# Optimization experiments

Measured on AMD Instinct MI355X. Metric: run time of the kernel, lower is better.

Reference implementation:

```python
import jax, jax.numpy as jnp
import numpy as np

N_HEAD, D_HEAD, D_MODEL = 8, 64, 512
QLEN, MLEN, BSZ = 1024, 1024, 4
KLEN = QLEN + MLEN
SCALE = 1.0 / (D_HEAD ** 0.5)
LN_EPS = 1e-5


def _rel_shift(x):
    # x: [qlen, rlen, bsz, n_head]
    q, rl, b, n = x.shape
    zero_pad = jnp.zeros((q, 1, b, n), x.dtype)
    x_padded = jnp.concatenate([zero_pad, x], axis=1).reshape(rl + 1, q, b, n)
    return x_padded[1:].reshape(q, rl, b, n)


def _layer_norm(x, g, b):
    mu = jnp.mean(x, axis=-1, keepdims=True)
    var = jnp.var(x, axis=-1, keepdims=True)
    return (x - mu) * jax.lax.rsqrt(var + LN_EPS) * g + b


def setup_inputs() -> dict:
    key = jax.random.key(0)
    ks = jax.random.split(key, 10)
    s = 0.02
    return {
        "w": jax.random.normal(ks[0], (QLEN, BSZ, D_MODEL), jnp.float32),
        "r": jax.random.normal(ks[1], (KLEN, 1, D_MODEL), jnp.float32),
        "r_w_bias": jax.random.normal(ks[2], (N_HEAD, D_HEAD), jnp.float32) * s,
        "r_r_bias": jax.random.normal(ks[3], (N_HEAD, D_HEAD), jnp.float32) * s,
        "mems": jax.random.normal(ks[4], (MLEN, BSZ, D_MODEL), jnp.float32),
        "Wq": jax.random.normal(ks[5], (D_MODEL, N_HEAD * D_HEAD), jnp.float32) * s,
        "Wkv": jax.random.normal(ks[6], (D_MODEL, 2 * N_HEAD * D_HEAD), jnp.float32) * s,
        "Wr": jax.random.normal(ks[7], (D_MODEL, N_HEAD * D_HEAD), jnp.float32) * s,
        "Wo": jax.random.normal(ks[8], (N_HEAD * D_HEAD, D_MODEL), jnp.float32) * s,
        "ln_g": jnp.ones((D_MODEL,), jnp.float32),
        "ln_b": jnp.zeros((D_MODEL,), jnp.float32),
        # causal mask: query i can attend keys j <= i + MLEN
        "attn_mask": jnp.arange(KLEN)[None, :] > (jnp.arange(QLEN) + MLEN)[:, None],
    }


def reference(w, r, r_w_bias, r_r_bias, mems, Wq, Wkv, Wr, Wo, ln_g, ln_b, attn_mask):
    qlen, bsz = w.shape[0], w.shape[1]
    cat = jnp.concatenate([mems, w], axis=0)          # [klen, bsz, d_model]
    klen = cat.shape[0]

    r_head_k = (r[:, 0] @ Wr).reshape(-1, N_HEAD, D_HEAD)   # [rlen, n, d]
    kv = cat @ Wkv                                           # [klen, bsz, 2*n*d]
    w_head_k, w_head_v = jnp.split(kv, 2, axis=-1)
    w_head_q = (cat[-qlen:] @ Wq).reshape(qlen, bsz, N_HEAD, D_HEAD)
    w_head_k = w_head_k.reshape(klen, bsz, N_HEAD, D_HEAD)
    w_head_v = w_head_v.reshape(klen, bsz, N_HEAD, D_HEAD)

    AC = jnp.einsum('ibnd,jbnd->ijbn', w_head_q + r_w_bias, w_head_k)
    BD = jnp.einsum('ibnd,jnd->ijbn', w_head_q + r_r_bias, r_head_k)
    BD = _rel_shift(BD)[:, :klen]

    attn_score = (AC + BD) * SCALE                           # [qlen, klen, bsz, n]
    attn_score = jnp.where(attn_mask[:, :, None, None], -jnp.inf, attn_score)
    attn_prob = jax.nn.softmax(attn_score, axis=1)

    attn_vec = jnp.einsum('ijbn,jbnd->ibnd', attn_prob, w_head_v)
    attn_vec = attn_vec.reshape(qlen, bsz, N_HEAD * D_HEAD)
    attn_out = attn_vec @ Wo
    return _layer_norm(w + attn_out, ln_g, ln_b)
```

## Files before the change

### kernel.cpp

```cpp
#include <hip/hip_runtime.h>
#include <hip/hip_bf16.h>
#include <math.h>

#define QLEN 1024
#define MLEN 1024
#define KLEN 2048
#define BSZ 4
#define NH 8
#define DH 64
#define DM 512
#define SCALE 0.125f
#define LN_EPS 1e-5f

#define RK_ROWS 2112

typedef __attribute__((ext_vector_type(8))) short short8;
typedef __attribute__((ext_vector_type(4))) float float4_;

#define GLB(p) ((const __attribute__((address_space(1))) void*)(p))
#define LDSP(p) ((__attribute__((address_space(3))) void*)(p))

__device__ inline ushort to_bf16(float x) {
  __hip_bfloat16 h = __float2bfloat16(x);
  return *reinterpret_cast<ushort*>(&h);
}

__device__ inline float row_max16(float v) {
  int x = __builtin_bit_cast(int, v);
  v = fmaxf(v, __builtin_bit_cast(float, __builtin_amdgcn_update_dpp(x, x, 0xB1, 0xF, 0xF, false)));
  x = __builtin_bit_cast(int, v);
  v = fmaxf(v, __builtin_bit_cast(float, __builtin_amdgcn_update_dpp(x, x, 0x4E, 0xF, 0xF, false)));
  x = __builtin_bit_cast(int, v);
  v = fmaxf(v, __builtin_bit_cast(float, __builtin_amdgcn_update_dpp(x, x, 0x124, 0xF, 0xF, false)));
  x = __builtin_bit_cast(int, v);
  v = fmaxf(v, __builtin_bit_cast(float, __builtin_amdgcn_update_dpp(x, x, 0x128, 0xF, 0xF, false)));
  return v;
}
__device__ inline float row_sum16(float v) {
  int x = __builtin_bit_cast(int, v);
  v += __builtin_bit_cast(float, __builtin_amdgcn_update_dpp(x, x, 0xB1, 0xF, 0xF, false));
  x = __builtin_bit_cast(int, v);
  v += __builtin_bit_cast(float, __builtin_amdgcn_update_dpp(x, x, 0x4E, 0xF, 0xF, false));
  x = __builtin_bit_cast(int, v);
  v += __builtin_bit_cast(float, __builtin_amdgcn_update_dpp(x, x, 0x124, 0xF, 0xF, false));
  x = __builtin_bit_cast(int, v);
  v += __builtin_bit_cast(float, __builtin_amdgcn_update_dpp(x, x, 0x128, 0xF, 0xF, false));
  return v;
}

__global__ __launch_bounds__(256) void wtrans_all(
    const float* __restrict__ Wq, const float* __restrict__ Wkv,
    const float* __restrict__ Wr, const float* __restrict__ Wo,
    ushort* __restrict__ WqT, ushort* __restrict__ WkvT,
    ushort* __restrict__ WrT, ushort* __restrict__ WoT) {
  __shared__ ushort tile[32][33];
  const int z = blockIdx.z;
  const float* W;
  ushort* WT;
  int N;
  if (z == 0)      { W = Wq;  WT = WqT;  N = DM; }
  else if (z == 1) { W = Wkv; WT = WkvT; N = 2 * DM; }
  else if (z == 2) { W = Wr;  WT = WrT;  N = DM; }
  else             { W = Wo;  WT = WoT;  N = DM; }
  const int k0 = blockIdx.x * 32, n0 = blockIdx.y * 32;
  if (n0 >= N) return;
  const int tid = threadIdx.x;
#pragma unroll
  for (int it = 0; it < 4; ++it) {
    int idx = tid + it * 256;
    int r = idx >> 5, c = idx & 31;
    tile[r][c] = to_bf16(W[(size_t)(k0 + r) * N + n0 + c]);
  }
  __syncthreads();
#pragma unroll
  for (int it = 0; it < 4; ++it) {
    int idx = tid + it * 256;
    int r = idx >> 5, c = idx & 31;
    WT[(size_t)(n0 + r) * DM + k0 + c] = tile[c][r];
  }
}

__global__ __launch_bounds__(256) void proj_all(
    const float* __restrict__ w, const float* __restrict__ mems,
    const float* __restrict__ r,
    const ushort* __restrict__ WqT, const ushort* __restrict__ WkvT,
    const ushort* __restrict__ WrT,
    const float* __restrict__ bias0, const float* __restrict__ bias1,
    ushort* __restrict__ qw, ushort* __restrict__ qr,
    ushort* __restrict__ k2, ushort* __restrict__ v2,
    ushort* __restrict__ rk2) {
  __shared__ ushort As[128 * 32];
  __shared__ ushort Bs[128 * 32];
  const int tid = threadIdx.x;
  int mode, bx, by;
  {
    int id = blockIdx.x;
    if (id < 128)      { mode = 0; bx = id >> 2;         by = id & 3; }
    else if (id < 640) { mode = 1; bx = (id - 128) >> 3; by = (id - 128) & 7; }
    else               { mode = 2; bx = (id - 640) >> 2; by = (id - 640) & 3; }
  }
  const int m0 = bx * 128, n0 = by * 128;
  const int wv = tid >> 6, lane = tid & 63;
  const int wm = wv >> 1, wn = wv & 1;
  const int l16 = lane & 15, quad = lane >> 4;

  const int arow = tid >> 1;
  const int acol = (tid & 1) * 16;
  const float* asrc;
  {
    int m = m0 + arow;
    if (mode == 2) asrc = r + (size_t)m * DM;
    else asrc = (m < QLEN * BSZ) ? w + (size_t)m * DM
                                 : mems + (size_t)(m - QLEN * BSZ) * DM;
    asrc += acol;
  }
  const ushort* BT = (mode == 0) ? WqT : (mode == 1) ? WkvT : WrT;
  const ushort* bsrc = BT + (size_t)(n0 + arow) * DM + acol;

  float4_ acc[4][4];
#pragma unroll
  for (int a = 0; a < 4; ++a)
#pragma unroll
    for (int b = 0; b < 4; ++b) acc[a][b] = float4_{0.f, 0.f, 0.f, 0.f};

  for (int k0 = 0; k0 < DM; k0 += 32) {
    float4 a0 = *reinterpret_cast<const float4*>(asrc + k0);
    float4 a1 = *reinterpret_cast<const float4*>(asrc + k0 + 4);
    float4 a2 = *reinterpret_cast<const float4*>(asrc + k0 + 8);
    float4 a3 = *reinterpret_cast<const float4*>(asrc + k0 + 12);
    ushort4 u0, u1, u2, u3;
    u0.x = to_bf16(a0.x); u0.y = to_bf16(a0.y); u0.z = to_bf16(a0.z); u0.w = to_bf16(a0.w);
    u1.x = to_bf16(a1.x); u1.y = to_bf16(a1.y); u1.z = to_bf16(a1.z); u1.w = to_bf16(a1.w);
    u2.x = to_bf16(a2.x); u2.y = to_bf16(a2.y); u2.z = to_bf16(a2.z); u2.w = to_bf16(a2.w);
    u3.x = to_bf16(a3.x); u3.y = to_bf16(a3.y); u3.z = to_bf16(a3.z); u3.w = to_bf16(a3.w);
    *reinterpret_cast<ushort4*>(&As[arow * 32 + acol]) = u0;
    *reinterpret_cast<ushort4*>(&As[arow * 32 + acol + 4]) = u1;
    *reinterpret_cast<ushort4*>(&As[arow * 32 + acol + 8]) = u2;
    *reinterpret_cast<ushort4*>(&As[arow * 32 + acol + 12]) = u3;
    *reinterpret_cast<uint4*>(&Bs[arow * 32 + acol]) =
        *reinterpret_cast<const uint4*>(bsrc + k0);
    *reinterpret_cast<uint4*>(&Bs[arow * 32 + acol + 8]) =
        *reinterpret_cast<const uint4*>(bsrc + k0 + 8);
    __syncthreads();
    short8 af[4], bf[4];
#pragma unroll
    for (int f = 0; f < 4; ++f) {
      af[f] = *reinterpret_cast<const short8*>(&As[(wm * 64 + f * 16 + l16) * 32 + quad * 8]);
      bf[f] = *reinterpret_cast<const short8*>(&Bs[(wn * 64 + f * 16 + l16) * 32 + quad * 8]);
    }
#pragma unroll
    for (int fm = 0; fm < 4; ++fm)
#pragma unroll
      for (int fn = 0; fn < 4; ++fn)
        acc[fm][fn] = __builtin_amdgcn_mfma_f32_16x16x32_bf16(bf[fn], af[fm], acc[fm][fn], 0, 0, 0);
    __syncthreads();
  }

#pragma unroll
  for (int fm = 0; fm < 4; ++fm) {
#pragma unroll
    for (int fn = 0; fn < 4; ++fn) {
      const int mm = m0 + wm * 64 + fm * 16 + l16;
      const int nnb = n0 + wn * 64 + fn * 16 + quad * 4;
      const float4_ a = acc[fm][fn];
      if (mode == 0) {
        float4 b0v = *reinterpret_cast<const float4*>(bias0 + nnb);
        float4 b1v = *reinterpret_cast<const float4*>(bias1 + nnb);
        int i = mm >> 2, b = mm & 3;
        int hd = nnb >> 6, d0 = nnb & 63;
        size_t idx = (((size_t)(b * NH + hd)) * QLEN + i) * DH + d0;
        ushort4 o0, o1;
        o0.x = to_bf16(a[0] + b0v.x); o0.y = to_bf16(a[1] + b0v.y);
        o0.z = to_bf16(a[2] + b0v.z); o0.w = to_bf16(a[3] + b0v.w);
        o1.x = to_bf16(a[0] + b1v.x); o1.y = to_bf16(a[1] + b1v.y);
        o1.z = to_bf16(a[2] + b1v.z); o1.w = to_bf16(a[3] + b1v.w);
        *reinterpret_cast<ushort4*>(qw + idx) = o0;
        *reinterpret_cast<ushort4*>(qr + idx) = o1;
      } else if (mode == 1) {
        int pos = mm >> 2, b = mm & 3;
        int jb = pos >> 5, jj = pos & 31;
        if (nnb < DM) {
          int hd = nnb >> 6, d = nnb & 63;
          int bn = b * NH + hd;
          int tile = ((jj >> 4) << 1) | (d >> 5);
          int lane2 = (((d >> 3) & 3) << 4) | (jj & 15);
          ushort4 o;
          o.x = to_bf16(a[0]); o.y = to_bf16(a[1]);
          o.z = to_bf16(a[2]); o.w = to_bf16(a[3]);
          *reinterpret_cast<ushort4*>(
              k2 + ((((size_t)bn * 64 + jb) * 4 + tile) * 64 + lane2) * 8 + (d & 7)) = o;
        } else {
          int nn2 = nnb - DM;
          int hd = nn2 >> 6, d = nn2 & 63;
          int bn = b * NH + hd;
          int tile = d >> 4;
          size_t base = ((((size_t)bn * 64 + jb) * 4 + tile) * 64 +
                         ((jj >> 3) << 4)) * 8 + (jj & 7);
#pragma unroll
          for (int reg = 0; reg < 4; ++reg)
            v2[base + (size_t)((d & 15) + reg) * 8] = to_bf16(a[reg]);
        }
      } else {
        int t = mm;
        int hd = nnb >> 6, d = nnb & 63;
        int cb = d >> 3;
        int dcol = ((cb ^ (t & 7)) << 3) | (d & 7);
        ushort4 o;
        o.x = to_bf16(a[0]); o.y = to_bf16(a[1]);
        o.z = to_bf16(a[2]); o.w = to_bf16(a[3]);
        *reinterpret_cast<ushort4*>(
            rk2 + ((size_t)hd * RK_ROWS + t) * DH + dcol) = o;
      }
    }
  }
}

__global__ __launch_bounds__(256) void mfma_out(
    const ushort* __restrict__ A, const ushort* __restrict__ BT,
    float* __restrict__ Y) {
  __shared__ ushort As[128 * 32];
  __shared__ ushort Bs[128 * 32];
  const int tid = threadIdx.x;
  const int m0 = blockIdx.x * 128, n0 = blockIdx.y * 128;
  const int wv = tid >> 6, lane = tid & 63;
  const int wm = wv >> 1, wn = wv & 1;
  const int l16 = lane & 15, quad = lane >> 4;
  const int arow = tid >> 1;
  const int acol = (tid & 1) * 16;
  const ushort* asrc = A + (size_t)(m0 + arow) * DM + acol;
  const ushort* bsrc = BT + (size_t)(n0 + arow) * DM + acol;

  float4_ acc[4][4];
#pragma unroll
  for (int a = 0; a < 4; ++a)
#pragma unroll
    for (int b = 0; b < 4; ++b) acc[a][b] = float4_{0.f, 0.f, 0.f, 0.f};

  for (int k0 = 0; k0 < DM; k0 += 32) {
    *reinterpret_cast<uint4*>(&As[arow * 32 + acol]) = *reinterpret_cast<const uint4*>(asrc + k0);
    *reinterpret_cast<uint4*>(&As[arow * 32 + acol + 8]) = *reinterpret_cast<const uint4*>(asrc + k0 + 8);
    *reinterpret_cast<uint4*>(&Bs[arow * 32 + acol]) = *reinterpret_cast<const uint4*>(bsrc + k0);
    *reinterpret_cast<uint4*>(&Bs[arow * 32 + acol + 8]) = *reinterpret_cast<const uint4*>(bsrc + k0 + 8);
    __syncthreads();
    short8 af[4], bf[4];
#pragma unroll
    for (int f = 0; f < 4; ++f) {
      af[f] = *reinterpret_cast<const short8*>(&As[(wm * 64 + f * 16 + l16) * 32 + quad * 8]);
      bf[f] = *reinterpret_cast<const short8*>(&Bs[(wn * 64 + f * 16 + l16) * 32 + quad * 8]);
    }
#pragma unroll
    for (int fm = 0; fm < 4; ++fm)
#pragma unroll
      for (int fn = 0; fn < 4; ++fn)
        acc[fm][fn] = __builtin_amdgcn_mfma_f32_16x16x32_bf16(bf[fn], af[fm], acc[fm][fn], 0, 0, 0);
    __syncthreads();
  }
#pragma unroll
  for (int fm = 0; fm < 4; ++fm)
#pragma unroll
    for (int fn = 0; fn < 4; ++fn) {
      int mm = m0 + wm * 64 + fm * 16 + l16;
      int nnb = n0 + wn * 64 + fn * 16 + quad * 4;
      float4 o;
      o.x = acc[fm][fn][0]; o.y = acc[fm][fn][1];
      o.z = acc[fm][fn][2]; o.w = acc[fm][fn][3];
      *reinterpret_cast<float4*>(Y + (size_t)mm * DM + nnb) = o;
    }
}

__global__ __launch_bounds__(256) void ln_fuse(
    const float* __restrict__ y, const float* __restrict__ wres,
    const float* __restrict__ g, const float* __restrict__ bb,
    float* __restrict__ out) {
  const int row = blockIdx.x * 4 + (threadIdx.x >> 6);
  const int lane = threadIdx.x & 63;
  const float* yr = y + (size_t)row * DM + lane * 4;
  const float* wr = wres + (size_t)row * DM + lane * 4;
  float4 x0 = *(const float4*)yr;
  float4 x1 = *(const float4*)(yr + 256);
  float4 w0 = *(const float4*)wr;
  float4 w1 = *(const float4*)(wr + 256);
  x0.x += w0.x; x0.y += w0.y; x0.z += w0.z; x0.w += w0.w;
  x1.x += w1.x; x1.y += w1.y; x1.z += w1.z; x1.w += w1.w;
  float s = x0.x + x0.y + x0.z + x0.w + x1.x + x1.y + x1.z + x1.w;
  float ss = x0.x * x0.x + x0.y * x0.y + x0.z * x0.z + x0.w * x0.w +
             x1.x * x1.x + x1.y * x1.y + x1.z * x1.z + x1.w * x1.w;
#pragma unroll
  for (int off = 1; off <= 32; off <<= 1) {
    s += __shfl_xor(s, off, 64);
    ss += __shfl_xor(ss, off, 64);
  }
  float mu = s * (1.f / DM);
  float var = ss * (1.f / DM) - mu * mu;
  float rstd = rsqrtf(var + LN_EPS);
  float4 g0 = *(const float4*)(g + lane * 4);
  float4 g1 = *(const float4*)(g + lane * 4 + 256);
  float4 b0 = *(const float4*)(bb + lane * 4);
  float4 b1 = *(const float4*)(bb + lane * 4 + 256);
  float4 o0, o1;
  o0.x = (x0.x - mu) * rstd * g0.x + b0.x;
  o0.y = (x0.y - mu) * rstd * g0.y + b0.y;
  o0.z = (x0.z - mu) * rstd * g0.z + b0.z;
  o0.w = (x0.w - mu) * rstd * g0.w + b0.w;
  o1.x = (x1.x - mu) * rstd * g1.x + b1.x;
  o1.y = (x1.y - mu) * rstd * g1.y + b1.y;
  o1.z = (x1.z - mu) * rstd * g1.z + b1.z;
  o1.w = (x1.w - mu) * rstd * g1.w + b1.w;
  float* orow = out + (size_t)row * DM + lane * 4;
  *reinterpret_cast<float4*>(orow) = o0;
  *reinterpret_cast<float4*>(orow + 256) = o1;
}

__global__ __launch_bounds__(256) void attn_mfma(
    const ushort* __restrict__ qw, const ushort* __restrict__ qr,
    const ushort* __restrict__ k2, const ushort* __restrict__ v2,
    const ushort* __restrict__ rk2, ushort* __restrict__ avbf) {
  const int i0b = (gridDim.x - 1 - blockIdx.x) * 64;
  const int n = blockIdx.y, b = blockIdx.z;
  const int bn = b * NH + n;
  const int tid = threadIdx.x;
  const int wv = tid >> 6, lane = tid & 63;
  const int l16 = lane & 15, quad = lane >> 4;
  const int i0w = i0b + wv * 16;

  __shared__ ushort stage[2][20 * 512];
  __shared__ float Dlds[4][16 * 66];
  __shared__ ushort Plds[4][16 * 32];
  float* __restrict__ Dw = Dlds[wv];
  ushort* __restrict__ Pw = Plds[wv];

  const ushort* __restrict__ k2b = k2 + (size_t)bn * (64 * 4 * 512);
  const ushort* __restrict__ v2b = v2 + (size_t)bn * (64 * 4 * 512);
  const ushort* __restrict__ rk2n = rk2 + (size_t)n * RK_ROWS * DH;

  const int nIter = (i0b + 63 + MLEN) / 32 + 1;

  short8 aqw0, aqw1, aqr0, aqr1;
  {
    const ushort* qwp = qw + (((size_t)bn * QLEN) + i0w + l16) * DH + quad * 8;
    const ushort* qrp = qr + (((size_t)bn * QLEN) + i0w + l16) * DH + quad * 8;
    aqw0 = *(const short8*)(qwp);
    aqw1 = *(const short8*)(qwp + 32);
    aqr0 = *(const short8*)(qrp);
    aqr1 = *(const short8*)(qrp + 32);
  }

  auto issue_dma = [&](int jb, int buf) {
    const int tbase = jb * 32 - i0b + 960;
#pragma unroll
    for (int s = 0; s < 5; ++s) {
      const int m = wv + s * 4;
      const ushort* g;
      if (m < 8) {
        const ushort* base = (m < 4) ? k2b : v2b;
        g = base + ((size_t)jb * 4 + (m & 3)) * 512 + lane * 8;
      } else {
        int tr = tbase + (m - 8) * 8 + (lane >> 3);
        g = rk2n + (size_t)tr * DH + (lane & 7) * 8;
      }
      __builtin_amdgcn_global_load_lds(GLB(g), LDSP(&stage[buf][m * 512]), 16, 0, 0);
    }
  };

  float4_ O[4];
#pragma unroll
  for (int t = 0; t < 4; ++t) O[t] = float4_{0.f, 0.f, 0.f, 0.f};
  float mrow[4] = {-INFINITY, -INFINITY, -INFINITY, -INFINITY};
  float lpart[4] = {0.f, 0.f, 0.f, 0.f};
  const float SL2E = SCALE * 1.44269504088896f;
  const int rbase = 48 - 16 * wv;
  const int sw = (l16 & 7);

  issue_dma(0, 0);
  issue_dma(1 < nIter ? 1 : 0, 1);

  for (int k = 0; k < nIter; ++k) {
    __builtin_amdgcn_s_waitcnt(0x0F75);
    __builtin_amdgcn_sched_barrier(0);
    __builtin_amdgcn_s_barrier();
    __builtin_amdgcn_sched_barrier(0);
    const ushort* sb = stage[k & 1];
    const int j0 = k * 32;

    float4_ ac[2];
#pragma unroll
    for (int h = 0; h < 2; ++h) {
      short8 b0 = *(const short8*)(sb + (h * 2 + 0) * 512 + lane * 8);
      short8 b1 = *(const short8*)(sb + (h * 2 + 1) * 512 + lane * 8);
      float4_ c = {0.f, 0.f, 0.f, 0.f};
      c = __builtin_amdgcn_mfma_f32_16x16x32_bf16(aqw0, b0, c, 0, 0, 0);
      c = __builtin_amdgcn_mfma_f32_16x16x32_bf16(aqw1, b1, c, 0, 0, 0);
      ac[h] = c;
    }
#pragma unroll
    for (int tt = 0; tt < 3; ++tt) {
      int rowLoc = rbase + tt * 16 + l16;
      const ushort* rrow = sb + 4096 + rowLoc * 64;
      short8 b0 = *(const short8*)(rrow + (((0 + quad) ^ sw) << 3));
      short8 b1 = *(const short8*)(rrow + (((4 + quad) ^ sw) << 3));
      float4_ d = {0.f, 0.f, 0.f, 0.f};
      d = __builtin_amdgcn_mfma_f32_16x16x32_bf16(aqr0, b0, d, 0, 0, 0);
      d = __builtin_amdgcn_mfma_f32_16x16x32_bf16(aqr1, b1, d, 0, 0, 0);
#pragma unroll
      for (int rg = 0; rg < 4; ++rg) {
        int row = quad * 4 + rg;
        Dw[row * 66 + tt * 16 + l16 + row] = d[rg];
      }
    }
    float s[2][4];
#pragma unroll
    for (int half = 0; half < 2; ++half) {
#pragma unroll
      for (int rg = 0; rg < 4; ++rg) {
        int row = quad * 4 + rg;
        int jloc = half * 16 + l16;
        float bd = Dw[row * 66 + jloc + 15];
        float sv = (ac[half][rg] + bd) * SL2E;
        s[half][rg] = (j0 + jloc > i0w + row + MLEN) ? -INFINITY : sv;
      }
    }
#pragma unroll
    for (int rg = 0; rg < 4; ++rg) {
      float mx = row_max16(fmaxf(s[0][rg], s[1][rg]));
      float mn = fmaxf(mrow[rg], mx);
      float alpha = __builtin_amdgcn_exp2f(mrow[rg] - mn);
      float p0 = __builtin_amdgcn_exp2f(s[0][rg] - mn);
      float p1 = __builtin_amdgcn_exp2f(s[1][rg] - mn);
      lpart[rg] = lpart[rg] * alpha + (p0 + p1);
      mrow[rg] = mn;
#pragma unroll
      for (int t = 0; t < 4; ++t) O[t][rg] *= alpha;
      int row = quad * 4 + rg;
      int idx0 = (l16 >> 3) * 128 + row * 8 + (l16 & 7);
      Pw[idx0] = to_bf16(p0);
      Pw[idx0 + 256] = to_bf16(p1);
    }
    short8 pfrag = *(const short8*)(Pw + lane * 8);
#pragma unroll
    for (int t = 0; t < 4; ++t) {
      short8 vfrag = *(const short8*)(sb + (4 + t) * 512 + lane * 8);
      O[t] = __builtin_amdgcn_mfma_f32_16x16x32_bf16(pfrag, vfrag, O[t], 0, 0, 0);
    }

    __builtin_amdgcn_sched_barrier(0);
    __builtin_amdgcn_s_barrier();
    __builtin_amdgcn_sched_barrier(0);
    int jn = k + 2;
    if (jn > nIter - 1) jn = nIter - 1;
    issue_dma(jn, k & 1);
  }

  float inv[4];
#pragma unroll
  for (int rg = 0; rg < 4; ++rg) inv[rg] = 1.f / row_sum16(lpart[rg]);
#pragma unroll
  for (int t = 0; t < 4; ++t)
#pragma unroll
    for (int rg = 0; rg < 4; ++rg) {
      int row = quad * 4 + rg;
      avbf[((size_t)(i0w + row) * BSZ + b) * DM + n * DH + t * 16 + l16] =
          to_bf16(O[t][rg] * inv[rg]);
    }
}

extern "C" void kernel_launch(void* const* d_in, const int* in_sizes, int n_in,
                              void* d_out, int out_size, void* d_ws, size_t ws_size,
                              hipStream_t stream) {
  const float* w    = (const float*)d_in[0];
  const float* r    = (const float*)d_in[1];
  const float* rwb  = (const float*)d_in[2];
  const float* rrb  = (const float*)d_in[3];
  const float* mems = (const float*)d_in[4];
  const float* Wq   = (const float*)d_in[5];
  const float* Wkv  = (const float*)d_in[6];
  const float* Wr   = (const float*)d_in[7];
  const float* Wo   = (const float*)d_in[8];
  const float* ln_g = (const float*)d_in[9];
  const float* ln_b = (const float*)d_in[10];
  float* out = (float*)d_out;

  char* p = (char*)d_ws;
  auto alloc = [&](size_t bytes) {
    char* q = p;
    p += (bytes + 255) & ~(size_t)255;
    return q;
  };
  ushort* WqT   = (ushort*)alloc((size_t)DM * DM * 2);
  ushort* WkvT  = (ushort*)alloc((size_t)2 * DM * DM * 2);
  ushort* WrT   = (ushort*)alloc((size_t)DM * DM * 2);
  ushort* WoT   = (ushort*)alloc((size_t)DM * DM * 2);
  ushort* qw    = (ushort*)alloc((size_t)BSZ * NH * QLEN * DH * 2);
  ushort* qr    = (ushort*)alloc((size_t)BSZ * NH * QLEN * DH * 2);
  ushort* k2    = (ushort*)alloc((size_t)BSZ * NH * 64 * 4 * 512 * 2);
  ushort* v2    = (ushort*)alloc((size_t)BSZ * NH * 64 * 4 * 512 * 2);
  ushort* rk2   = (ushort*)alloc((size_t)NH * RK_ROWS * DH * 2);
  ushort* avbf  = (ushort*)alloc((size_t)QLEN * BSZ * DM * 2);
  float* y = (float*)k2;

  wtrans_all<<<dim3(16, 32, 4), dim3(256), 0, stream>>>(
      Wq, Wkv, Wr, Wo, WqT, WkvT, WrT, WoT);
  proj_all<<<dim3(704), dim3(256), 0, stream>>>(
      w, mems, r, WqT, WkvT, WrT, rwb, rrb, qw, qr, k2, v2, rk2);
  attn_mfma<<<dim3(QLEN / 64, NH, BSZ), dim3(256), 0, stream>>>(qw, qr, k2, v2, rk2, avbf);
  mfma_out<<<dim3(32, 4), dim3(256), 0, stream>>>(avbf, WoT, y);
  ln_fuse<<<dim3(QLEN * BSZ / 4), dim3(256), 0, stream>>>(y, w, ln_g, ln_b, out);
}
```

Baseline: 253.6 us.

## Split attention over key range into two segments and merge with combine kernel

Each attention block now handles half of the key range, doubling the grid, and writes unnormalized bf16 partial outputs plus per-row max and sum. A new combine kernel merges the two partials into the final attention vector. The relative-position key fragments are now read straight from global memory into registers instead of being staged in LDS, so their swizzle is removed and LDS use shrinks. Occupancy is hinted at four blocks per CU. The aim is more parallelism and better load balance across the causal triangle, at the cost of an extra kernel launch, extra partial-output traffic and bf16 rounding of the partials.

```diff
diff --git a/kernel.cpp b/kernel.cpp
--- a/kernel.cpp
+++ b/kernel.cpp
@@ -23,6 +23,11 @@
 __device__ inline ushort to_bf16(float x) {
   __hip_bfloat16 h = __float2bfloat16(x);
   return *reinterpret_cast<ushort*>(&h);
+}
+__device__ inline float bf16_to_f(ushort u) {
+  union { unsigned int i; float f; } v;
+  v.i = (unsigned int)u << 16;
+  return v.f;
 }
 
 __device__ inline float row_max16(float v) {
@@ -203,13 +208,11 @@
       } else {
         int t = mm;
         int hd = nnb >> 6, d = nnb & 63;
-        int cb = d >> 3;
-        int dcol = ((cb ^ (t & 7)) << 3) | (d & 7);
         ushort4 o;
         o.x = to_bf16(a[0]); o.y = to_bf16(a[1]);
         o.z = to_bf16(a[2]); o.w = to_bf16(a[3]);
         *reinterpret_cast<ushort4*>(
-            rk2 + ((size_t)hd * RK_ROWS + t) * DH + dcol) = o;
+            rk2 + ((size_t)hd * RK_ROWS + t) * DH + d) = o;
       }
     }
   }
@@ -311,19 +314,21 @@
   *reinterpret_cast<float4*>(orow + 256) = o1;
 }
 
-__global__ __launch_bounds__(256) void attn_mfma(
+__global__ __launch_bounds__(256, 4) void attn_mfma(
     const ushort* __restrict__ qw, const ushort* __restrict__ qr,
     const ushort* __restrict__ k2, const ushort* __restrict__ v2,
-    const ushort* __restrict__ rk2, ushort* __restrict__ avbf) {
+    const ushort* __restrict__ rk2, ushort* __restrict__ Opart,
+    float* __restrict__ ml) {
   const int i0b = (gridDim.x - 1 - blockIdx.x) * 64;
-  const int n = blockIdx.y, b = blockIdx.z;
+  const int n = blockIdx.y;
+  const int b = blockIdx.z >> 1, seg = blockIdx.z & 1;
   const int bn = b * NH + n;
   const int tid = threadIdx.x;
   const int wv = tid >> 6, lane = tid & 63;
   const int l16 = lane & 15, quad = lane >> 4;
   const int i0w = i0b + wv * 16;
 
-  __shared__ ushort stage[2][20 * 512];
+  __shared__ ushort stage[2][8 * 512];
   __shared__ float Dlds[4][16 * 66];
   __shared__ ushort Plds[4][16 * 32];
   float* __restrict__ Dw = Dlds[wv];
@@ -333,7 +338,10 @@
   const ushort* __restrict__ v2b = v2 + (size_t)bn * (64 * 4 * 512);
   const ushort* __restrict__ rk2n = rk2 + (size_t)n * RK_ROWS * DH;
 
-  const int nIter = (i0b + 63 + MLEN) / 32 + 1;
+  const int nIterTot = (i0b + 63 + MLEN) / 32 + 1;
+  const int nHalf = nIterTot >> 1;
+  const int c0 = seg ? nHalf : 0;
+  const int c1 = seg ? nIterTot : nHalf;
 
   short8 aqw0, aqw1, aqr0, aqr1;
   {
@@ -346,18 +354,11 @@
   }
 
   auto issue_dma = [&](int jb, int buf) {
-    const int tbase = jb * 32 - i0b + 960;
-#pragma unroll
-    for (int s = 0; s < 5; ++s) {
+#pragma unroll
+    for (int s = 0; s < 2; ++s) {
       const int m = wv + s * 4;
-      const ushort* g;
-      if (m < 8) {
-        const ushort* base = (m < 4) ? k2b : v2b;
-        g = base + ((size_t)jb * 4 + (m & 3)) * 512 + lane * 8;
-      } else {
-        int tr = tbase + (m - 8) * 8 + (lane >> 3);
-        g = rk2n + (size_t)tr * DH + (lane & 7) * 8;
-      }
+      const ushort* base = (m < 4) ? k2b : v2b;
+      const ushort* g = base + ((size_t)jb * 4 + (m & 3)) * 512 + lane * 8;
       __builtin_amdgcn_global_load_lds(GLB(g), LDSP(&stage[buf][m * 512]), 16, 0, 0);
     }
   };
@@ -369,18 +370,26 @@
   float lpart[4] = {0.f, 0.f, 0.f, 0.f};
   const float SL2E = SCALE * 1.44269504088896f;
   const int rbase = 48 - 16 * wv;
-  const int sw = (l16 & 7);
-
-  issue_dma(0, 0);
-  issue_dma(1 < nIter ? 1 : 0, 1);
-
-  for (int k = 0; k < nIter; ++k) {
-    __builtin_amdgcn_s_waitcnt(0x0F75);
+
+  issue_dma(c0, 0);
+  issue_dma(c0 + 1, 1);
+
+  for (int k = c0; k < c1; ++k) {
+    __builtin_amdgcn_s_waitcnt(0x0F72);
     __builtin_amdgcn_sched_barrier(0);
     __builtin_amdgcn_s_barrier();
     __builtin_amdgcn_sched_barrier(0);
     const ushort* sb = stage[k & 1];
     const int j0 = k * 32;
+
+    const int tbase = j0 - i0b + 960;
+    short8 rb0[3], rb1[3];
+#pragma unroll
+    for (int tt = 0; tt < 3; ++tt) {
+      const ushort* rrow = rk2n + (size_t)(tbase + rbase + tt * 16 + l16) * DH;
+      rb0[tt] = *(const short8*)(rrow + quad * 8);
+      rb1[tt] = *(const short8*)(rrow + (4 + quad) * 8);
+    }
 
     float4_ ac[2];
 #pragma unroll
@@ -394,13 +403,9 @@
     }
 #pragma unroll
     for (int tt = 0; tt < 3; ++tt) {
-      int rowLoc = rbase + tt * 16 + l16;
-      const ushort* rrow = sb + 4096 + rowLoc * 64;
-      short8 b0 = *(const short8*)(rrow + (((0 + quad) ^ sw) << 3));
-      short8 b1 = *(const short8*)(rrow + (((4 + quad) ^ sw) << 3));
       float4_ d = {0.f, 0.f, 0.f, 0.f};
-      d = __builtin_amdgcn_mfma_f32_16x16x32_bf16(aqr0, b0, d, 0, 0, 0);
-      d = __builtin_amdgcn_mfma_f32_16x16x32_bf16(aqr1, b1, d, 0, 0, 0);
+      d = __builtin_amdgcn_mfma_f32_16x16x32_bf16(aqr0, rb0[tt], d, 0, 0, 0);
+      d = __builtin_amdgcn_mfma_f32_16x16x32_bf16(aqr1, rb1[tt], d, 0, 0, 0);
 #pragma unroll
       for (int rg = 0; rg < 4; ++rg) {
         int row = quad * 4 + rg;
@@ -446,21 +451,52 @@
     __builtin_amdgcn_s_barrier();
     __builtin_amdgcn_sched_barrier(0);
     int jn = k + 2;
-    if (jn > nIter - 1) jn = nIter - 1;
+    if (jn > c1 - 1) jn = c1 - 1;
     issue_dma(jn, k & 1);
   }
 
-  float inv[4];
-#pragma unroll
-  for (int rg = 0; rg < 4; ++rg) inv[rg] = 1.f / row_sum16(lpart[rg]);
-#pragma unroll
-  for (int t = 0; t < 4; ++t)
-#pragma unroll
-    for (int rg = 0; rg < 4; ++rg) {
-      int row = quad * 4 + rg;
-      avbf[((size_t)(i0w + row) * BSZ + b) * DM + n * DH + t * 16 + l16] =
-          to_bf16(O[t][rg] * inv[rg]);
-    }
+  float lsum[4];
+#pragma unroll
+  for (int rg = 0; rg < 4; ++rg) lsum[rg] = row_sum16(lpart[rg]);
+  ushort* op = Opart + (size_t)seg * QLEN * BSZ * DM;
+  float2* mlp = (float2*)ml;
+#pragma unroll
+  for (int rg = 0; rg < 4; ++rg) {
+    int row = quad * 4 + rg;
+    if (l16 == 0) {
+      mlp[((size_t)seg * QLEN * BSZ + (size_t)(i0w + row) * BSZ + b) * NH + n] =
+          float2{mrow[rg], lsum[rg]};
+    }
+#pragma unroll
+    for (int t = 0; t < 4; ++t) {
+      op[((size_t)(i0w + row) * BSZ + b) * DM + n * DH + t * 16 + l16] =
+          to_bf16(O[t][rg]);
+    }
+  }
+}
+
+__global__ __launch_bounds__(256) void attn_combine(
+    const ushort* __restrict__ Opart, const float* __restrict__ ml,
+    ushort* __restrict__ avbf) {
+  const int row = blockIdx.x;
+  const int tid = threadIdx.x;
+  const int col = tid * 2;
+  const int h = col >> 6;
+  const float2* mlp = (const float2*)ml;
+  float2 a = mlp[(size_t)row * NH + h];
+  float2 c = mlp[((size_t)QLEN * BSZ + row) * NH + h];
+  float M = fmaxf(a.x, c.x);
+  float e0 = __builtin_amdgcn_exp2f(a.x - M);
+  float e1 = __builtin_amdgcn_exp2f(c.x - M);
+  float inv = 1.f / (a.y * e0 + c.y * e1);
+  float s0 = e0 * inv, s1 = e1 * inv;
+  size_t base = (size_t)row * DM + col;
+  ushort2 o0 = *(const ushort2*)(Opart + base);
+  ushort2 o1 = *(const ushort2*)(Opart + (size_t)QLEN * BSZ * DM + base);
+  ushort2 o;
+  o.x = to_bf16(bf16_to_f(o0.x) * s0 + bf16_to_f(o1.x) * s1);
+  o.y = to_bf16(bf16_to_f(o0.y) * s0 + bf16_to_f(o1.y) * s1);
+  *(ushort2*)(avbf + base) = o;
 }
 
 extern "C" void kernel_launch(void* const* d_in, const int* in_sizes, int n_in,
@@ -495,13 +531,17 @@
   ushort* v2    = (ushort*)alloc((size_t)BSZ * NH * 64 * 4 * 512 * 2);
   ushort* rk2   = (ushort*)alloc((size_t)NH * RK_ROWS * DH * 2);
   ushort* avbf  = (ushort*)alloc((size_t)QLEN * BSZ * DM * 2);
+  ushort* Opart = (ushort*)alloc((size_t)2 * QLEN * BSZ * DM * 2);
+  float*  ml    = (float*)alloc((size_t)2 * QLEN * BSZ * NH * 2 * 4);
   float* y = (float*)k2;
 
   wtrans_all<<<dim3(16, 32, 4), dim3(256), 0, stream>>>(
       Wq, Wkv, Wr, Wo, WqT, WkvT, WrT, WoT);
   proj_all<<<dim3(704), dim3(256), 0, stream>>>(
       w, mems, r, WqT, WkvT, WrT, rwb, rrb, qw, qr, k2, v2, rk2);
-  attn_mfma<<<dim3(QLEN / 64, NH, BSZ), dim3(256), 0, stream>>>(qw, qr, k2, v2, rk2, avbf);
+  attn_mfma<<<dim3(QLEN / 64, NH, BSZ * 2), dim3(256), 0, stream>>>(
+      qw, qr, k2, v2, rk2, Opart, ml);
+  attn_combine<<<dim3(QLEN * BSZ), dim3(256), 0, stream>>>(Opart, ml, avbf);
   mfma_out<<<dim3(32, 4), dim3(256), 0, stream>>>(avbf, WoT, y);
   ln_fuse<<<dim3(QLEN * BSZ / 4), dim3(256), 0, stream>>>(y, w, ln_g, ln_b, out);
 }
```

Result: slower. 260.6 us (+2.8%).
